# Performance work log

Hardware: AMD Instinct MI355X
Metric: run time of the kernel (lower is better)

## Reference

```python
import jax, jax.numpy as jnp
from jax import lax
import numpy as np

B, T, D, H = 64, 2048, 4, 256
ALPHA, WINDOW = 0.5, 64


def _make_binom(alpha, w):
    # (-1)^j * C(alpha, j) for j = 0..w (Grunwald-Letnikov coefficients)
    coeffs = []
    for j in range(w + 1):
        c = 1.0
        for i in range(j):
            c *= (alpha - i) / (i + 1)
        coeffs.append(((-1.0) ** j) * c)
    return jnp.asarray(np.array(coeffs, dtype=np.float32))


def setup_inputs() -> dict:
    key = jax.random.key(0)
    ks = jax.random.split(key, 12)
    x = jax.random.normal(ks[0], (B, T, D), dtype=jnp.float32)
    # time channel (index 3) must be monotonically increasing for time_diff**alpha
    time = jnp.arange(T, dtype=jnp.float32) * 0.1
    x = x.at[:, :, 3].set(jnp.broadcast_to(time, (B, T)))
    s = 0.05
    f32 = jnp.float32
    return {
        "x": x,
        "Wih0": s * jax.random.normal(ks[1], (H, D), f32),
        "Whh0": s * jax.random.normal(ks[2], (H, H), f32),
        "bih0": jnp.zeros((H,), f32),
        "bhh0": jnp.zeros((H,), f32),
        "Wih1": s * jax.random.normal(ks[3], (H, H), f32),
        "Whh1": s * jax.random.normal(ks[4], (H, H), f32),
        "bih1": jnp.zeros((H,), f32),
        "bhh1": jnp.zeros((H,), f32),
        "fcW": s * jax.random.normal(ks[5], (1, H), f32),
        "fcb": jnp.zeros((1,), f32),
        "Q": jnp.asarray(2.9, f32),
        "delta": jnp.asarray(1.0, f32),
        "f1W": s * jax.random.normal(ks[6], (H, 1), f32),
        "f1b": jnp.zeros((H,), f32),
        "f2W": s * jax.random.normal(ks[7], (1, H), f32),
        "f2b": jnp.zeros((1,), f32),
        "U0": jnp.asarray(1.0, f32),
        "R0": jnp.asarray(1.0, f32),
        "C1": jnp.asarray(1.0, f32),
        "R1": jnp.asarray(1.0, f32),
        "binom": _make_binom(ALPHA, WINDOW),
    }


def reference(x, Wih0, Whh0, bih0, bhh0, Wih1, Whh1, bih1, bhh1,
              fcW, fcb, Q, delta, f1W, f1b, f2W, f2b, U0, R0, C1, R1, binom):
    Bsz, Tlen, _ = x.shape

    def soc_fn(xx):
        xs = jnp.swapaxes(xx, 0, 1)  # [T, B, D]
        h0 = jnp.zeros((Bsz, Wih0.shape[0]), xx.dtype)

        def cell(Wih, Whh, bih, bhh):
            def f(h, xt):
                h = jnp.tanh(xt @ Wih.T + bih + h @ Whh.T + bhh)
                return h, h
            return f

        _, ys1 = lax.scan(cell(Wih0, Whh0, bih0, bhh0), h0, xs)  # [T, B, H]
        hT, _ = lax.scan(cell(Wih1, Whh1, bih1, bhh1), h0, ys1)  # [B, H]
        return hT @ fcW.T + fcb  # [B, 1]

    soc = soc_fn(x)
    # d soc / d x at last timestep, last feature (torch autograd.grad with ones grad_outputs)
    d_soc = jax.grad(lambda xx: soc_fn(xx).sum())(x)[:, -1, -1]  # [B]
    loss1 = delta / Q * x[:, -1, 1:2] + d_soc  # [B,1]+[B] -> [B,B] (matches torch broadcast)

    f_soc = (soc @ f1W.T + f1b) @ f2W.T + f2b  # [B, 1]

    # fractional-order windowed Up sequence (vectorized over t)
    v = x[:, :, 0]
    I = x[:, :, 1]
    time = x[:, :, 3]
    t_idx = jnp.arange(Tlen)
    start = jnp.maximum(0, t_idx - WINDOW + 1)
    valid = t_idx + 1 - start  # window length at each t
    tdiff = jnp.where(valid > 1,
                      (time - time[:, start]) / jnp.maximum(valid - 1, 1).astype(x.dtype),
                      jnp.asarray(1.0, x.dtype))  # [B, T]
    Ts = tdiff ** ALPHA
    # history_sum[t] = sum_{m=0}^{w-1} binom[w-m] * v[t-m] == causal conv with kernel binom[1:w+1]
    kern = binom[1:WINDOW + 1]
    hist = lax.conv_general_dilated(v[:, None, :], kern[None, None, :],
                                    (1,), [(WINDOW - 1, 0)])[:, 0, :]  # [B, T]
    Up = (-Ts / (R1 * C1)) * v + (Ts / C1) * I - hist  # [B, T]

    loss2 = f_soc - x[:, -1, 0:1] - R0 * x[:, -1, 1:2] - Up[:, -1]  # [B,1]-[B] -> [B,B]
    return (soc, loss1, loss2)
```

## Files before the change

### kernel.cpp

```cpp
#include <hip/hip_runtime.h>


#define TT 2048
#define HH 256
#define WIN 64

typedef uint uvec32 __attribute__((ext_vector_type(32)));

#if __has_builtin(__builtin_amdgcn_sdot4)
__device__ __forceinline__ int sdot4(uint a, uint b, int c) {
  return __builtin_amdgcn_sdot4((int)a, (int)b, c, false);
}
#else
__device__ __forceinline__ int sdot4(uint a, uint b, int c) {
#pragma unroll
  for (int k = 0; k < 4; ++k) {
    int av = (int)(a << (24 - 8 * k)) >> 24;
    int bv = (int)(b << (24 - 8 * k)) >> 24;
    c += av * bv;
  }
  return c;
}
#endif

__device__ __forceinline__ float tanh_fast(float x) {
  float xc = fminf(fmaxf(x, -15.f), 15.f);
  float e = __expf(2.f * xc);
  return (e - 1.f) * __builtin_amdgcn_rcpf(e + 1.f);
}

__device__ __forceinline__ float block_sum8(float v, float* red, int tid) {
#pragma unroll
  for (int off = 32; off >= 1; off >>= 1) v += __shfl_down(v, off, 64);
  __syncthreads();
  if ((tid & 63) == 0) red[tid >> 6] = v;
  __syncthreads();
  float s = 0.f;
#pragma unroll
  for (int w = 0; w < 8; ++w) s += red[w];
  return s;
}

__device__ __forceinline__ float max_half(const float* __restrict__ base) {
  const float4* g = (const float4*)base;
  float m = 0.f;
#pragma unroll
  for (int i = 0; i < 32; ++i) {
    float4 a = g[i];
    m = fmaxf(m, fmaxf(fmaxf(fabsf(a.x), fabsf(a.y)),
                       fmaxf(fabsf(a.z), fabsf(a.w))));
  }
  return m;
}

__device__ __forceinline__ uvec32 quant_half(const float* __restrict__ base,
                                             float inv) {
  uvec32 w;
  const float4* g = (const float4*)base;
#pragma unroll
  for (int i = 0; i < 32; ++i) {
    float4 a = g[i];
    int b0 = (int)rintf(a.x * inv), b1 = (int)rintf(a.y * inv);
    int b2 = (int)rintf(a.z * inv), b3 = (int)rintf(a.w * inv);
    w[i] = (uint)(b0 & 0xFF) | ((uint)(b1 & 0xFF) << 8) |
           ((uint)(b2 & 0xFF) << 16) | ((uint)(b3 & 0xFF) << 24);
  }
  return w;
}

#define IDOTHALF(WV, HP, ACC)                                              \
  {                                                                        \
    _Pragma("unroll") for (int _i = 0; _i < 8; ++_i) {                     \
      uint4 _u = (HP)[_i];                                                 \
      ACC = sdot4(WV[4 * _i + 0], _u.x, ACC);                              \
      ACC = sdot4(WV[4 * _i + 1], _u.y, ACC);                              \
      ACC = sdot4(WV[4 * _i + 2], _u.z, ACC);                              \
      ACC = sdot4(WV[4 * _i + 3], _u.w, ACC);                              \
    }                                                                      \
  }

__global__ __launch_bounds__(512) void rnn_chain_kernel(
    const float* __restrict__ x, const float* __restrict__ Wih0,
    const float* __restrict__ Whh0, const float* __restrict__ bih0,
    const float* __restrict__ bhh0, const float* __restrict__ Wih1,
    const float* __restrict__ Whh1, const float* __restrict__ bih1,
    const float* __restrict__ bhh1, const float* __restrict__ fcW,
    const float* __restrict__ fcb, const float* __restrict__ f1W,
    const float* __restrict__ f1b, const float* __restrict__ f2W,
    const float* __restrict__ f2b, const float* __restrict__ C1,
    const float* __restrict__ R1, const float* __restrict__ binom,
    float* __restrict__ out_soc,
    float* __restrict__ ws)
{
  const int b = blockIdx.x;
  const int tid = threadIdx.x;
  const int j = tid & 255;
  const int half = tid >> 8;

  __shared__ __align__(16) float xs[TT * 4];
  __shared__ __align__(16) uint qh0L[HH / 4];
  __shared__ __align__(16) uint qh1L[HH / 4];
  __shared__ float fpZ0[2 * HH];
  __shared__ float fpZ1[2 * HH];
  __shared__ float sMax[3][2][HH];
  __shared__ float red[8];
  __shared__ float uL[HH];

  const float4* xg = (const float4*)(x + (size_t)b * TT * 4);
  float4* xl = (float4*)xs;
  for (int i = tid; i < TT; i += 512) xl[i] = xg[i];

  const size_t roff = (size_t)j * HH + half * 128;
  sMax[0][half][j] = max_half(Whh0 + roff);
  sMax[1][half][j] = max_half(Wih1 + roff);
  sMax[2][half][j] = max_half(Whh1 + roff);
  __syncthreads();
  const float m0 = fmaxf(sMax[0][0][j], sMax[0][1][j]);
  const float m1 = fmaxf(sMax[1][0][j], sMax[1][1][j]);
  const float m2 = fmaxf(sMax[2][0][j], sMax[2][1][j]);
  const float F0 = m0 * (1.f / 16129.f);
  const float F1i = m1 * (1.f / 16129.f);
  const float F1h = m2 * (1.f / 16129.f);
  const uvec32 w0 = quant_half(Whh0 + roff, m0 > 0.f ? 127.f / m0 : 0.f);
  const uvec32 w1i = quant_half(Wih1 + roff, m1 > 0.f ? 127.f / m1 : 0.f);
  const uvec32 w1h = quant_half(Whh1 + roff, m2 > 0.f ? 127.f / m2 : 0.f);

  const float4 wx = ((const float4*)Wih0)[j];
  const float mybias = half ? (bih1[j] + bhh1[j]) : (bih0[j] + bhh0[j]);

  __syncthreads();

  if (half == 0) {
    float4 x0v = xl[0];
    float h00 = tanh_fast(wx.x * x0v.x + wx.y * x0v.y + wx.z * x0v.z +
                          wx.w * x0v.w + mybias);
    ((char*)qh0L)[j] = (char)(int)rintf(h00 * 127.f);
  }
  if (tid < HH / 4) qh1L[tid] = 0u;
  __syncthreads();

  const uint4* h0p = (const uint4*)qh0L + half * 8;
  const uint4* h1p = (const uint4*)qh1L + half * 8;

  float myhT = 0.f;

  for (int t = 0; t < TT - 1; ++t) {
    int C = 0, E = 0, A = 0;
    IDOTHALF(w1h, h1p, C);
#pragma unroll
    for (int i = 0; i < 8; ++i) {
      uint4 u = h0p[i];
      E = sdot4(w1i[4 * i + 0], u.x, E);
      A = sdot4(w0[4 * i + 0], u.x, A);
      E = sdot4(w1i[4 * i + 1], u.y, E);
      A = sdot4(w0[4 * i + 1], u.y, A);
      E = sdot4(w1i[4 * i + 2], u.z, E);
      A = sdot4(w0[4 * i + 2], u.z, A);
      E = sdot4(w1i[4 * i + 3], u.w, E);
      A = sdot4(w0[4 * i + 3], u.w, A);
    }
    fpZ1[half * HH + j] = F1i * (float)E + F1h * (float)C;
    fpZ0[half * HH + j] = F0 * (float)A;
    __syncthreads();
    if (half == 1) {
      float z1 = fpZ1[j] + fpZ1[HH + j] + mybias;
      myhT = tanh_fast(z1);
      ((char*)qh1L)[j] = (char)(int)rintf(myhT * 127.f);
    } else {
      float4 xt = xl[t + 1];
      float z0 = fpZ0[j] + fpZ0[HH + j] + wx.x * xt.x + wx.y * xt.y +
                 wx.z * xt.z + wx.w * xt.w + mybias;
      myhT = tanh_fast(z0);
      ((char*)qh0L)[j] = (char)(int)rintf(myhT * 127.f);
    }
    __syncthreads();
  }

  {
    int C = 0, E = 0;
    IDOTHALF(w1h, h1p, C);
    IDOTHALF(w1i, h0p, E);
    fpZ1[half * HH + j] = F1i * (float)E + F1h * (float)C;
    __syncthreads();
    if (half == 1) {
      float z1 = fpZ1[j] + fpZ1[HH + j] + mybias;
      myhT = tanh_fast(z1);
    }
    __syncthreads();
  }

  const float fw = fcW[j];

  float socb = block_sum8(half == 1 ? fw * myhT : 0.f, red, tid) + fcb[0];
  if (tid == 0) out_soc[b] = socb;

  float fsv = (half == 1) ? f2W[j] * (socb * f1W[j] + f1b[j]) : 0.f;
  float fsb = block_sum8(fsv, red, tid) + f2b[0];
  if (tid == 0) ws[64 + b] = fsb;

  if (half == 1) uL[j] = fw * (1.f - myhT * myhT);
  __syncthreads();
  float g = 0.f;
  {
    const int k0 = half * 128;
#pragma unroll 8
    for (int k = 0; k < 128; ++k)
      g += uL[k0 + k] * Wih1[(size_t)(k0 + k) * HH + j];
  }
  if (half == 1) fpZ0[j] = g;
  __syncthreads();
  float dsv = 0.f;
  if (half == 0) dsv = (g + fpZ0[j]) * (1.f - myhT * myhT) * wx.w;
  float dsoc = block_sum8(dsv, red, tid);
  if (tid == 0) ws[b] = dsoc;

  float histv = 0.f;
  if (tid < WIN) histv = binom[tid + 1] * xs[(TT - WIN + tid) * 4 + 0];
  float hist = block_sum8(histv, red, tid);
  if (tid == 0) {
    float tl = xs[(TT - 1) * 4 + 3], t0v = xs[(TT - WIN) * 4 + 3];
    float tdiff = (tl - t0v) * (1.0f / (float)(WIN - 1));
    float Ts = sqrtf(tdiff);
    float vlast = xs[(TT - 1) * 4 + 0], Ilast = xs[(TT - 1) * 4 + 1];
    float r1 = R1[0], c1v = C1[0];
    float up = -Ts / (r1 * c1v) * vlast + Ts / c1v * Ilast - hist;
    ws[128 + b] = up;
  }
}

__global__ void assemble_kernel(const float* __restrict__ x,
                                const float* __restrict__ Q,
                                const float* __restrict__ delta,
                                const float* __restrict__ R0,
                                const float* __restrict__ ws,
                                float* __restrict__ out) {
  const int i = blockIdx.x;
  const int jj = threadIdx.x;
  const float dq = delta[0] / Q[0];
  const size_t base = ((size_t)i * TT + (TT - 1)) * 4;
  const float xv0 = x[base + 0];
  const float xv1 = x[base + 1];
  const float fs = ws[64 + i];
  out[64 + i * 64 + jj] = dq * xv1 + ws[jj];
  out[64 + 4096 + i * 64 + jj] = fs - xv0 - R0[0] * xv1 - ws[128 + jj];
}

extern "C" void kernel_launch(void* const* d_in, const int* in_sizes, int n_in,
                              void* d_out, int out_size, void* d_ws,
                              size_t ws_size, hipStream_t stream) {
  const float* x    = (const float*)d_in[0];
  const float* Wih0 = (const float*)d_in[1];
  const float* Whh0 = (const float*)d_in[2];
  const float* bih0 = (const float*)d_in[3];
  const float* bhh0 = (const float*)d_in[4];
  const float* Wih1 = (const float*)d_in[5];
  const float* Whh1 = (const float*)d_in[6];
  const float* bih1 = (const float*)d_in[7];
  const float* bhh1 = (const float*)d_in[8];
  const float* fcW  = (const float*)d_in[9];
  const float* fcb  = (const float*)d_in[10];
  const float* Q    = (const float*)d_in[11];
  const float* delta= (const float*)d_in[12];
  const float* f1W  = (const float*)d_in[13];
  const float* f1b  = (const float*)d_in[14];
  const float* f2W  = (const float*)d_in[15];
  const float* f2b  = (const float*)d_in[16];
  const float* R0   = (const float*)d_in[18];
  const float* C1   = (const float*)d_in[19];
  const float* R1   = (const float*)d_in[20];
  const float* binom= (const float*)d_in[21];

  float* out = (float*)d_out;
  float* ws  = (float*)d_ws;

  hipLaunchKernelGGL(rnn_chain_kernel, dim3(64), dim3(512), 0, stream, x,
                     Wih0, Whh0, bih0, bhh0, Wih1, Whh1, bih1, bhh1, fcW, fcb,
                     f1W, f1b, f2W, f2b, C1, R1, binom, out, ws);
  hipLaunchKernelGGL(assemble_kernel, dim3(64), dim3(64), 0, stream, x, Q,
                     delta, R0, ws, out);
}
```

Baseline: 1.812 ms.

## Split recurrent dot products over four thread groups and precompute input projections

The block grows from 512 to 1024 threads, so each hidden unit's int8 dot products are split four ways instead of two. Each thread now holds 16 packed weight words per matrix instead of 32, which eases register pressure. Integer partial sums go to shared memory and are reduced by the owning quarter. The layer-0 input projection is computed once for all timesteps into a global workspace and prefetched two steps ahead, taking it off the sequential critical path. In exchange, each step reads more shared memory, barriers now span 16 waves, and the workspace needs about 128 MB of global memory.

```diff
diff --git a/kernel.cpp b/kernel.cpp
--- a/kernel.cpp
+++ b/kernel.cpp
@@ -5,7 +5,7 @@
 #define HH 256
 #define WIN 64
 
-typedef uint uvec32 __attribute__((ext_vector_type(32)));
+typedef uint uvec16 __attribute__((ext_vector_type(16)));
 
 #if __has_builtin(__builtin_amdgcn_sdot4)
 __device__ __forceinline__ int sdot4(uint a, uint b, int c) {
@@ -29,7 +29,7 @@
   return (e - 1.f) * __builtin_amdgcn_rcpf(e + 1.f);
 }
 
-__device__ __forceinline__ float block_sum8(float v, float* red, int tid) {
+__device__ __forceinline__ float block_sum16(float v, float* red, int tid) {
 #pragma unroll
   for (int off = 32; off >= 1; off >>= 1) v += __shfl_down(v, off, 64);
   __syncthreads();
@@ -37,15 +37,15 @@
   __syncthreads();
   float s = 0.f;
 #pragma unroll
-  for (int w = 0; w < 8; ++w) s += red[w];
+  for (int w = 0; w < 16; ++w) s += red[w];
   return s;
 }
 
-__device__ __forceinline__ float max_half(const float* __restrict__ base) {
+__device__ __forceinline__ float max_quarter(const float* __restrict__ base) {
   const float4* g = (const float4*)base;
   float m = 0.f;
 #pragma unroll
-  for (int i = 0; i < 32; ++i) {
+  for (int i = 0; i < 16; ++i) {
     float4 a = g[i];
     m = fmaxf(m, fmaxf(fmaxf(fabsf(a.x), fabsf(a.y)),
                        fmaxf(fabsf(a.z), fabsf(a.w))));
@@ -53,12 +53,12 @@
   return m;
 }
 
-__device__ __forceinline__ uvec32 quant_half(const float* __restrict__ base,
-                                             float inv) {
-  uvec32 w;
+__device__ __forceinline__ uvec16 quant_quarter(const float* __restrict__ base,
+                                                float inv) {
+  uvec16 w;
   const float4* g = (const float4*)base;
 #pragma unroll
-  for (int i = 0; i < 32; ++i) {
+  for (int i = 0; i < 16; ++i) {
     float4 a = g[i];
     int b0 = (int)rintf(a.x * inv), b1 = (int)rintf(a.y * inv);
     int b2 = (int)rintf(a.z * inv), b3 = (int)rintf(a.w * inv);
@@ -68,18 +68,7 @@
   return w;
 }
 
-#define IDOTHALF(WV, HP, ACC)                                              \
-  {                                                                        \
-    _Pragma("unroll") for (int _i = 0; _i < 8; ++_i) {                     \
-      uint4 _u = (HP)[_i];                                                 \
-      ACC = sdot4(WV[4 * _i + 0], _u.x, ACC);                              \
-      ACC = sdot4(WV[4 * _i + 1], _u.y, ACC);                              \
-      ACC = sdot4(WV[4 * _i + 2], _u.z, ACC);                              \
-      ACC = sdot4(WV[4 * _i + 3], _u.w, ACC);                              \
-    }                                                                      \
-  }
-
-__global__ __launch_bounds__(512) void rnn_chain_kernel(
+__global__ __launch_bounds__(1024) void rnn_chain_kernel(
     const float* __restrict__ x, const float* __restrict__ Wih0,
     const float* __restrict__ Whh0, const float* __restrict__ bih0,
     const float* __restrict__ bhh0, const float* __restrict__ Wih1,
@@ -95,60 +84,92 @@
   const int b = blockIdx.x;
   const int tid = threadIdx.x;
   const int j = tid & 255;
-  const int half = tid >> 8;
+  const int q = tid >> 8;
 
   __shared__ __align__(16) float xs[TT * 4];
   __shared__ __align__(16) uint qh0L[HH / 4];
   __shared__ __align__(16) uint qh1L[HH / 4];
-  __shared__ float fpZ0[2 * HH];
-  __shared__ float fpZ1[2 * HH];
-  __shared__ float sMax[3][2][HH];
-  __shared__ float red[8];
+  __shared__ int pA_[4 * HH];
+  __shared__ int pE_[4 * HH];
+  __shared__ int pC_[4 * HH];
+  __shared__ float sMax[3][4][HH];
+  __shared__ float pF[4 * HH];
+  __shared__ float red[16];
   __shared__ float uL[HH];
 
   const float4* xg = (const float4*)(x + (size_t)b * TT * 4);
   float4* xl = (float4*)xs;
-  for (int i = tid; i < TT; i += 512) xl[i] = xg[i];
-
-  const size_t roff = (size_t)j * HH + half * 128;
-  sMax[0][half][j] = max_half(Whh0 + roff);
-  sMax[1][half][j] = max_half(Wih1 + roff);
-  sMax[2][half][j] = max_half(Whh1 + roff);
-  __syncthreads();
-  const float m0 = fmaxf(sMax[0][0][j], sMax[0][1][j]);
-  const float m1 = fmaxf(sMax[1][0][j], sMax[1][1][j]);
-  const float m2 = fmaxf(sMax[2][0][j], sMax[2][1][j]);
-  const float F0 = m0 * (1.f / 16129.f);
-  const float F1i = m1 * (1.f / 16129.f);
-  const float F1h = m2 * (1.f / 16129.f);
-  const uvec32 w0 = quant_half(Whh0 + roff, m0 > 0.f ? 127.f / m0 : 0.f);
-  const uvec32 w1i = quant_half(Wih1 + roff, m1 > 0.f ? 127.f / m1 : 0.f);
-  const uvec32 w1h = quant_half(Whh1 + roff, m2 > 0.f ? 127.f / m2 : 0.f);
-
-  const float4 wx = ((const float4*)Wih0)[j];
-  const float mybias = half ? (bih1[j] + bhh1[j]) : (bih0[j] + bhh0[j]);
-
-  __syncthreads();
-
-  if (half == 0) {
-    float4 x0v = xl[0];
-    float h00 = tanh_fast(wx.x * x0v.x + wx.y * x0v.y + wx.z * x0v.z +
-                          wx.w * x0v.w + mybias);
+  for (int i = tid; i < TT; i += 1024) xl[i] = xg[i];
+  __syncthreads();
+
+  float* xdb = ws + 1024 + (size_t)b * TT * HH;
+  float xd0 = 0.f, xd1 = 0.f;
+  {
+    const float4 wx = ((const float4*)Wih0)[j];
+    const float b0 = bih0[j] + bhh0[j];
+    const int t0 = q * (TT / 4);
+#pragma unroll 4
+    for (int t = t0; t < t0 + TT / 4; ++t) {
+      float4 xv = xl[t];
+      float d = wx.x * xv.x + wx.y * xv.y + wx.z * xv.z + wx.w * xv.w + b0;
+      xdb[(size_t)t * HH + j] = d;
+      if (t == 0) xd0 = d;
+      if (t == 1) xd1 = d;
+    }
+  }
+
+  const size_t roff = (size_t)j * HH + q * 64;
+  sMax[0][q][j] = max_quarter(Whh0 + roff);
+  sMax[1][q][j] = max_quarter(Wih1 + roff);
+  sMax[2][q][j] = max_quarter(Whh1 + roff);
+  __syncthreads();
+  const float m0 = fmaxf(fmaxf(sMax[0][0][j], sMax[0][1][j]),
+                         fmaxf(sMax[0][2][j], sMax[0][3][j]));
+  const float m1 = fmaxf(fmaxf(sMax[1][0][j], sMax[1][1][j]),
+                         fmaxf(sMax[1][2][j], sMax[1][3][j]));
+  const float m2 = fmaxf(fmaxf(sMax[2][0][j], sMax[2][1][j]),
+                         fmaxf(sMax[2][2][j], sMax[2][3][j]));
+
+  const uvec16 w0 = quant_quarter(Whh0 + roff, m0 > 0.f ? 127.f / m0 : 0.f);
+  const uvec16 w1i = quant_quarter(Wih1 + roff, m1 > 0.f ? 127.f / m1 : 0.f);
+  const uvec16 w1h = quant_quarter(Whh1 + roff, m2 > 0.f ? 127.f / m2 : 0.f);
+
+  const float F0 = (q == 0) ? m0 * (1.f / 16129.f) : 0.f;
+  const float F1i = (q == 1) ? m1 * (1.f / 16129.f) : 0.f;
+  const float F1h = (q == 1) ? m2 * (1.f / 16129.f) : 0.f;
+  const float bias1 = (q == 1) ? (bih1[j] + bhh1[j]) : 0.f;
+
+  if (q == 0) {
+    float h00 = tanh_fast(xd0);
     ((char*)qh0L)[j] = (char)(int)rintf(h00 * 127.f);
   }
   if (tid < HH / 4) qh1L[tid] = 0u;
-  __syncthreads();
-
-  const uint4* h0p = (const uint4*)qh0L + half * 8;
-  const uint4* h1p = (const uint4*)qh1L + half * 8;
+  float xdn = xd1;
+  __syncthreads();
+
+  const uint4* h0p = (const uint4*)qh0L + q * 4;
+  const uint4* h1p = (const uint4*)qh1L + q * 4;
 
   float myhT = 0.f;
 
   for (int t = 0; t < TT - 1; ++t) {
-    int C = 0, E = 0, A = 0;
-    IDOTHALF(w1h, h1p, C);
-#pragma unroll
-    for (int i = 0; i < 8; ++i) {
+    float xnn = 0.f;
+    if (q == 0) {
+      int idx = (t + 2 < TT) ? t + 2 : TT - 1;
+      xnn = xdb[(size_t)idx * HH + j];
+    }
+    int C = 0;
+#pragma unroll
+    for (int i = 0; i < 4; ++i) {
+      uint4 u = h1p[i];
+      C = sdot4(w1h[4 * i + 0], u.x, C);
+      C = sdot4(w1h[4 * i + 1], u.y, C);
+      C = sdot4(w1h[4 * i + 2], u.z, C);
+      C = sdot4(w1h[4 * i + 3], u.w, C);
+    }
+    int E = 0, A = 0;
+#pragma unroll
+    for (int i = 0; i < 4; ++i) {
       uint4 u = h0p[i];
       E = sdot4(w1i[4 * i + 0], u.x, E);
       A = sdot4(w0[4 * i + 0], u.x, A);
@@ -159,31 +180,56 @@
       E = sdot4(w1i[4 * i + 3], u.w, E);
       A = sdot4(w0[4 * i + 3], u.w, A);
     }
-    fpZ1[half * HH + j] = F1i * (float)E + F1h * (float)C;
-    fpZ0[half * HH + j] = F0 * (float)A;
+    pA_[q * HH + j] = A;
+    pE_[q * HH + j] = E;
+    pC_[q * HH + j] = C;
     __syncthreads();
-    if (half == 1) {
-      float z1 = fpZ1[j] + fpZ1[HH + j] + mybias;
+    if (q == 0) {
+      float z0 = F0 * (float)(pA_[j] + pA_[HH + j] + pA_[2 * HH + j] +
+                              pA_[3 * HH + j]) +
+                 xdn;
+      myhT = tanh_fast(z0);
+      ((char*)qh0L)[j] = (char)(int)rintf(myhT * 127.f);
+    } else if (q == 1) {
+      float z1 = F1i * (float)(pE_[j] + pE_[HH + j] + pE_[2 * HH + j] +
+                               pE_[3 * HH + j]) +
+                 F1h * (float)(pC_[j] + pC_[HH + j] + pC_[2 * HH + j] +
+                               pC_[3 * HH + j]) +
+                 bias1;
       myhT = tanh_fast(z1);
       ((char*)qh1L)[j] = (char)(int)rintf(myhT * 127.f);
-    } else {
-      float4 xt = xl[t + 1];
-      float z0 = fpZ0[j] + fpZ0[HH + j] + wx.x * xt.x + wx.y * xt.y +
-                 wx.z * xt.z + wx.w * xt.w + mybias;
-      myhT = tanh_fast(z0);
-      ((char*)qh0L)[j] = (char)(int)rintf(myhT * 127.f);
-    }
+    }
+    xdn = xnn;
     __syncthreads();
   }
 
   {
     int C = 0, E = 0;
-    IDOTHALF(w1h, h1p, C);
-    IDOTHALF(w1i, h0p, E);
-    fpZ1[half * HH + j] = F1i * (float)E + F1h * (float)C;
+#pragma unroll
+    for (int i = 0; i < 4; ++i) {
+      uint4 u = h1p[i];
+      C = sdot4(w1h[4 * i + 0], u.x, C);
+      C = sdot4(w1h[4 * i + 1], u.y, C);
+      C = sdot4(w1h[4 * i + 2], u.z, C);
+      C = sdot4(w1h[4 * i + 3], u.w, C);
+    }
+#pragma unroll
+    for (int i = 0; i < 4; ++i) {
+      uint4 u = h0p[i];
+      E = sdot4(w1i[4 * i + 0], u.x, E);
+      E = sdot4(w1i[4 * i + 1], u.y, E);
+      E = sdot4(w1i[4 * i + 2], u.z, E);
+      E = sdot4(w1i[4 * i + 3], u.w, E);
+    }
+    pE_[q * HH + j] = E;
+    pC_[q * HH + j] = C;
     __syncthreads();
-    if (half == 1) {
-      float z1 = fpZ1[j] + fpZ1[HH + j] + mybias;
+    if (q == 1) {
+      float z1 = F1i * (float)(pE_[j] + pE_[HH + j] + pE_[2 * HH + j] +
+                               pE_[3 * HH + j]) +
+                 F1h * (float)(pC_[j] + pC_[HH + j] + pC_[2 * HH + j] +
+                               pC_[3 * HH + j]) +
+                 bias1;
       myhT = tanh_fast(z1);
     }
     __syncthreads();
@@ -191,32 +237,36 @@
 
   const float fw = fcW[j];
 
-  float socb = block_sum8(half == 1 ? fw * myhT : 0.f, red, tid) + fcb[0];
+  float socb = block_sum16(q == 1 ? fw * myhT : 0.f, red, tid) + fcb[0];
   if (tid == 0) out_soc[b] = socb;
 
-  float fsv = (half == 1) ? f2W[j] * (socb * f1W[j] + f1b[j]) : 0.f;
-  float fsb = block_sum8(fsv, red, tid) + f2b[0];
+  float fsv = (q == 1) ? f2W[j] * (socb * f1W[j] + f1b[j]) : 0.f;
+  float fsb = block_sum16(fsv, red, tid) + f2b[0];
   if (tid == 0) ws[64 + b] = fsb;
 
-  if (half == 1) uL[j] = fw * (1.f - myhT * myhT);
-  __syncthreads();
-  float g = 0.f;
+  if (q == 1) uL[j] = fw * (1.f - myhT * myhT);
+  __syncthreads();
   {
-    const int k0 = half * 128;
+    float g = 0.f;
+    const int k0 = q * 64;
 #pragma unroll 8
-    for (int k = 0; k < 128; ++k)
+    for (int k = 0; k < 64; ++k)
       g += uL[k0 + k] * Wih1[(size_t)(k0 + k) * HH + j];
-  }
-  if (half == 1) fpZ0[j] = g;
+    pF[q * HH + j] = g;
+  }
   __syncthreads();
   float dsv = 0.f;
-  if (half == 0) dsv = (g + fpZ0[j]) * (1.f - myhT * myhT) * wx.w;
-  float dsoc = block_sum8(dsv, red, tid);
+  if (q == 0) {
+    float g = pF[j] + pF[HH + j] + pF[2 * HH + j] + pF[3 * HH + j];
+    float wx3 = Wih0[j * 4 + 3];
+    dsv = g * (1.f - myhT * myhT) * wx3;
+  }
+  float dsoc = block_sum16(dsv, red, tid);
   if (tid == 0) ws[b] = dsoc;
 
   float histv = 0.f;
   if (tid < WIN) histv = binom[tid + 1] * xs[(TT - WIN + tid) * 4 + 0];
-  float hist = block_sum8(histv, red, tid);
+  float hist = block_sum16(histv, red, tid);
   if (tid == 0) {
     float tl = xs[(TT - 1) * 4 + 3], t0v = xs[(TT - WIN) * 4 + 3];
     float tdiff = (tl - t0v) * (1.0f / (float)(WIN - 1));
@@ -273,7 +323,7 @@
   float* out = (float*)d_out;
   float* ws  = (float*)d_ws;
 
-  hipLaunchKernelGGL(rnn_chain_kernel, dim3(64), dim3(512), 0, stream, x,
+  hipLaunchKernelGGL(rnn_chain_kernel, dim3(64), dim3(1024), 0, stream, x,
                      Wih0, Whh0, bih0, bhh0, Wih1, Whh1, bih1, bhh1, fcW, fcb,
                      f1W, f1b, f2W, f2b, C1, R1, binom, out, ws);
   hipLaunchKernelGGL(assemble_kernel, dim3(64), dim3(64), 0, stream, x, Q,
```

Result: faster. 1.716 ms (-5.3%).

## Reduce RNN half-sums via wave shuffles and double-buffer hidden state to one barrier

Applied to the files above, without the earlier changes.

Thread mapping changes so that the two K-halves of each output row sit in the same wavefront (lanes j and j+32). Partial dot products are combined with __shfl_xor instead of an LDS round trip. Hidden-state buffers are double-buffered, so each timestep needs only one __syncthreads instead of two. Both halves now run tanh, with the layer-0 and layer-1 tails split by lane, which adds some redundant FMA work and divergence per wave.

```diff
diff --git a/kernel.cpp b/kernel.cpp
--- a/kernel.cpp
+++ b/kernel.cpp
@@ -67,17 +67,6 @@
   }
   return w;
 }
-
-#define IDOTHALF(WV, HP, ACC)                                              \
-  {                                                                        \
-    _Pragma("unroll") for (int _i = 0; _i < 8; ++_i) {                     \
-      uint4 _u = (HP)[_i];                                                 \
-      ACC = sdot4(WV[4 * _i + 0], _u.x, ACC);                              \
-      ACC = sdot4(WV[4 * _i + 1], _u.y, ACC);                              \
-      ACC = sdot4(WV[4 * _i + 2], _u.z, ACC);                              \
-      ACC = sdot4(WV[4 * _i + 3], _u.w, ACC);                              \
-    }                                                                      \
-  }
 
 __global__ __launch_bounds__(512) void rnn_chain_kernel(
     const float* __restrict__ x, const float* __restrict__ Wih0,
@@ -94,59 +83,70 @@
 {
   const int b = blockIdx.x;
   const int tid = threadIdx.x;
-  const int j = tid & 255;
-  const int half = tid >> 8;
+  const int lane = tid & 63;
+  const int wv = tid >> 6;
+  const int half = lane >> 5;
+  const int j = (wv << 5) | (lane & 31);
 
   __shared__ __align__(16) float xs[TT * 4];
-  __shared__ __align__(16) uint qh0L[HH / 4];
-  __shared__ __align__(16) uint qh1L[HH / 4];
-  __shared__ float fpZ0[2 * HH];
-  __shared__ float fpZ1[2 * HH];
-  __shared__ float sMax[3][2][HH];
+  __shared__ __align__(16) uint qh0L[2][HH / 4];
+  __shared__ __align__(16) uint qh1L[2][HH / 4];
   __shared__ float red[8];
   __shared__ float uL[HH];
+  __shared__ float s0L[HH];
+  __shared__ float pF[2 * HH];
 
   const float4* xg = (const float4*)(x + (size_t)b * TT * 4);
   float4* xl = (float4*)xs;
   for (int i = tid; i < TT; i += 512) xl[i] = xg[i];
 
   const size_t roff = (size_t)j * HH + half * 128;
-  sMax[0][half][j] = max_half(Whh0 + roff);
-  sMax[1][half][j] = max_half(Wih1 + roff);
-  sMax[2][half][j] = max_half(Whh1 + roff);
-  __syncthreads();
-  const float m0 = fmaxf(sMax[0][0][j], sMax[0][1][j]);
-  const float m1 = fmaxf(sMax[1][0][j], sMax[1][1][j]);
-  const float m2 = fmaxf(sMax[2][0][j], sMax[2][1][j]);
+  float mm0 = max_half(Whh0 + roff);
+  float mm1 = max_half(Wih1 + roff);
+  float mm2 = max_half(Whh1 + roff);
+  const float m0 = fmaxf(mm0, __shfl_xor(mm0, 32));
+  const float m1 = fmaxf(mm1, __shfl_xor(mm1, 32));
+  const float m2 = fmaxf(mm2, __shfl_xor(mm2, 32));
+
+  const uvec32 w0 = quant_half(Whh0 + roff, m0 > 0.f ? 127.f / m0 : 0.f);
+  const uvec32 w1i = quant_half(Wih1 + roff, m1 > 0.f ? 127.f / m1 : 0.f);
+  const uvec32 w1h = quant_half(Whh1 + roff, m2 > 0.f ? 127.f / m2 : 0.f);
+
   const float F0 = m0 * (1.f / 16129.f);
   const float F1i = m1 * (1.f / 16129.f);
   const float F1h = m2 * (1.f / 16129.f);
-  const uvec32 w0 = quant_half(Whh0 + roff, m0 > 0.f ? 127.f / m0 : 0.f);
-  const uvec32 w1i = quant_half(Wih1 + roff, m1 > 0.f ? 127.f / m1 : 0.f);
-  const uvec32 w1h = quant_half(Whh1 + roff, m2 > 0.f ? 127.f / m2 : 0.f);
-
   const float4 wx = ((const float4*)Wih0)[j];
-  const float mybias = half ? (bih1[j] + bhh1[j]) : (bih0[j] + bhh0[j]);
-
-  __syncthreads();
-
-  if (half == 0) {
+  const float bias0 = bih0[j] + bhh0[j];
+  const float bias1 = bih1[j] + bhh1[j];
+
+  __syncthreads();
+
+  {
     float4 x0v = xl[0];
-    float h00 = tanh_fast(wx.x * x0v.x + wx.y * x0v.y + wx.z * x0v.z +
-                          wx.w * x0v.w + mybias);
-    ((char*)qh0L)[j] = (char)(int)rintf(h00 * 127.f);
-  }
-  if (tid < HH / 4) qh1L[tid] = 0u;
-  __syncthreads();
-
-  const uint4* h0p = (const uint4*)qh0L + half * 8;
-  const uint4* h1p = (const uint4*)qh1L + half * 8;
-
-  float myhT = 0.f;
+    float xd = wx.x * x0v.x + wx.y * x0v.y + wx.z * x0v.z + wx.w * x0v.w +
+               bias0;
+    float h00 = tanh_fast(xd);
+    char* hb = half ? (char*)&qh1L[0][0] : (char*)&qh0L[0][0];
+    char v = half ? (char)0 : (char)(int)rintf(h00 * 127.f);
+    hb[j] = v;
+  }
+  __syncthreads();
+
+  int cur = 0;
+  float myh = 0.f;
 
   for (int t = 0; t < TT - 1; ++t) {
+    const uint4* h0p = (const uint4*)&qh0L[cur][0] + half * 8;
+    const uint4* h1p = (const uint4*)&qh1L[cur][0] + half * 8;
     int C = 0, E = 0, A = 0;
-    IDOTHALF(w1h, h1p, C);
+#pragma unroll
+    for (int i = 0; i < 8; ++i) {
+      uint4 u = h1p[i];
+      C = sdot4(w1h[4 * i + 0], u.x, C);
+      C = sdot4(w1h[4 * i + 1], u.y, C);
+      C = sdot4(w1h[4 * i + 2], u.z, C);
+      C = sdot4(w1h[4 * i + 3], u.w, C);
+    }
 #pragma unroll
     for (int i = 0; i < 8; ++i) {
       uint4 u = h0p[i];
@@ -159,58 +159,70 @@
       E = sdot4(w1i[4 * i + 3], u.w, E);
       A = sdot4(w0[4 * i + 3], u.w, A);
     }
-    fpZ1[half * HH + j] = F1i * (float)E + F1h * (float)C;
-    fpZ0[half * HH + j] = F0 * (float)A;
+    A += __shfl_xor(A, 32);
+    E += __shfl_xor(E, 32);
+    C += __shfl_xor(C, 32);
+    float4 xt = xl[t + 1];
+    float xd = wx.x * xt.x + wx.y * xt.y + wx.z * xt.z + wx.w * xt.w + bias0;
+    float z = half ? (F1i * (float)E + F1h * (float)C + bias1)
+                   : (F0 * (float)A + xd);
+    myh = tanh_fast(z);
+    char* hb = half ? (char*)&qh1L[cur ^ 1][0] : (char*)&qh0L[cur ^ 1][0];
+    hb[j] = (char)(int)rintf(myh * 127.f);
+    cur ^= 1;
     __syncthreads();
-    if (half == 1) {
-      float z1 = fpZ1[j] + fpZ1[HH + j] + mybias;
-      myhT = tanh_fast(z1);
-      ((char*)qh1L)[j] = (char)(int)rintf(myhT * 127.f);
-    } else {
-      float4 xt = xl[t + 1];
-      float z0 = fpZ0[j] + fpZ0[HH + j] + wx.x * xt.x + wx.y * xt.y +
-                 wx.z * xt.z + wx.w * xt.w + mybias;
-      myhT = tanh_fast(z0);
-      ((char*)qh0L)[j] = (char)(int)rintf(myhT * 127.f);
-    }
-    __syncthreads();
   }
 
   {
+    const uint4* h0p = (const uint4*)&qh0L[cur][0] + half * 8;
+    const uint4* h1p = (const uint4*)&qh1L[cur][0] + half * 8;
     int C = 0, E = 0;
-    IDOTHALF(w1h, h1p, C);
-    IDOTHALF(w1i, h0p, E);
-    fpZ1[half * HH + j] = F1i * (float)E + F1h * (float)C;
-    __syncthreads();
-    if (half == 1) {
-      float z1 = fpZ1[j] + fpZ1[HH + j] + mybias;
-      myhT = tanh_fast(z1);
-    }
-    __syncthreads();
+#pragma unroll
+    for (int i = 0; i < 8; ++i) {
+      uint4 u = h1p[i];
+      C = sdot4(w1h[4 * i + 0], u.x, C);
+      C = sdot4(w1h[4 * i + 1], u.y, C);
+      C = sdot4(w1h[4 * i + 2], u.z, C);
+      C = sdot4(w1h[4 * i + 3], u.w, C);
+    }
+#pragma unroll
+    for (int i = 0; i < 8; ++i) {
+      uint4 u = h0p[i];
+      E = sdot4(w1i[4 * i + 0], u.x, E);
+      E = sdot4(w1i[4 * i + 1], u.y, E);
+      E = sdot4(w1i[4 * i + 2], u.z, E);
+      E = sdot4(w1i[4 * i + 3], u.w, E);
+    }
+    E += __shfl_xor(E, 32);
+    C += __shfl_xor(C, 32);
+    if (half) myh = tanh_fast(F1i * (float)E + F1h * (float)C + bias1);
   }
 
   const float fw = fcW[j];
 
-  float socb = block_sum8(half == 1 ? fw * myhT : 0.f, red, tid) + fcb[0];
+  float socb = block_sum8(half ? fw * myh : 0.f, red, tid) + fcb[0];
   if (tid == 0) out_soc[b] = socb;
 
-  float fsv = (half == 1) ? f2W[j] * (socb * f1W[j] + f1b[j]) : 0.f;
+  float fsv = half ? f2W[j] * (socb * f1W[j] + f1b[j]) : 0.f;
   float fsb = block_sum8(fsv, red, tid) + f2b[0];
   if (tid == 0) ws[64 + b] = fsb;
 
-  if (half == 1) uL[j] = fw * (1.f - myhT * myhT);
-  __syncthreads();
-  float g = 0.f;
+  if (half) uL[j] = fw * (1.f - myh * myh);
+  else      s0L[j] = (1.f - myh * myh) * wx.w;
+  __syncthreads();
   {
-    const int k0 = half * 128;
+    const int h = tid & 255;
+    const int kh = tid >> 8;
+    float g = 0.f;
+    const int k0 = kh * 128;
 #pragma unroll 8
     for (int k = 0; k < 128; ++k)
-      g += uL[k0 + k] * Wih1[(size_t)(k0 + k) * HH + j];
-  }
-  if (half == 1) fpZ0[j] = g;
+      g += uL[k0 + k] * Wih1[(size_t)(k0 + k) * HH + h];
+    pF[kh * HH + h] = g;
+  }
   __syncthreads();
   float dsv = 0.f;
-  if (half == 0) dsv = (g + fpZ0[j]) * (1.f - myhT * myhT) * wx.w;
+  if (tid < HH) dsv = (pF[tid] + pF[HH + tid]) * s0L[tid];
   float dsoc = block_sum8(dsv, red, tid);
   if (tid == 0) ws[b] = dsoc;
 
```

After: 1.617 ms. 10.8% less time.
